# Performance work log

Measured on AMD Instinct MI355X. Metric: run time of the kernel, lower is better.

Reference implementation:

```python
import jax, jax.numpy as jnp
import numpy as np

WIN, OFFSET_D, TRUNC, SIGMA = 60, 40, 21, 9
EPS = 1e-8


def smoothing_filter():
    half = TRUNC // 2
    x = jnp.arange(-half, half + 1, dtype=jnp.float32)
    g = jnp.exp(-0.5 * (x / SIGMA) ** 2)
    g = g / g.sum()
    f = jnp.zeros(WIN, jnp.float32)
    c = WIN // 2
    return f.at[c - half:c + half + 1].set(g)


def setup_inputs() -> dict:
    key = jax.random.key(0)
    kx, kl, kt, kw = jax.random.split(key, 4)
    B, T, K = 64, 4000, 100
    X = jax.random.uniform(kx, (B, T, K), jnp.float32, 1e-4, 1.0 - 1e-4)
    lengths = jax.random.randint(kl, (B,), T // 2, T + 1, dtype=jnp.int32)
    tgt = jax.random.randint(kt, (B,), 0, K, dtype=jnp.int32)
    w_end = jax.random.randint(kw, (B,), 1, T // 2, dtype=jnp.int32)
    return {"X": X, "lengths": lengths, "tgt": tgt, "w_end": w_end}


def reference(X, lengths, tgt, w_end):
    B, T, K = X.shape
    filt = smoothing_filter()
    tau_s = jnp.maximum(0, w_end + OFFSET_D - WIN)      # (B,)
    tau_e = jnp.minimum(tau_s + WIN, lengths)           # (B,)
    t = jnp.arange(T)

    # ---- negative term: -log(1 - p) over all valid frames, excluding the
    # target keyword's pooling window [tau_s, tau_e) ----
    neg = -jnp.log(jnp.clip(1.0 - X, EPS, 1.0))                         # (B,T,K)
    len_mask = (t[None, :] < lengths[:, None]).astype(X.dtype)          # (B,T)
    win_mask = ((t[None, :] >= tau_s[:, None]) & (t[None, :] < tau_e[:, None])).astype(X.dtype)
    tgt_onehot = jax.nn.one_hot(tgt, K, dtype=X.dtype)                  # (B,K)
    neg_loss = jnp.sum(neg * len_mask[:, :, None]) - jnp.einsum('btk,bt,bk->', neg, win_mask, tgt_onehot)

    # ---- positive term: smoothed max pooling over window of target keyword ----
    prob_tgt = jnp.take_along_axis(X, tgt[:, None, None], axis=2)[..., 0]  # (B,T)
    win = jax.vmap(lambda p, s: jax.lax.dynamic_slice(p, (s,), (WIN,)))(prob_tgt, tau_s)
    Lw = tau_e - tau_s                                                   # valid window length
    pos = jnp.arange(WIN)
    valid = pos[None, :] < Lw[:, None]
    win = win * valid.astype(X.dtype)  # zero beyond valid length == zero-padded ragged conv
    total_pad = WIN - 1
    pl = total_pad // 2  # torch 'same': extra pad on the right
    smoothed = jax.lax.conv_general_dilated(
        win[:, None, :], filt[None, None, :], (1,), [(pl, total_pad - pl)])[:, 0, :]
    smoothed = jnp.clip(smoothed, EPS, 1.0)
    smoothed = jnp.where(valid, smoothed, 0.0)  # exclude out-of-window positions from max
    pos_loss = -jnp.log(smoothed.max(axis=1)).sum()

    return neg_loss + pos_loss
```

## Files before the change

kernel.cpp:

```cpp
#include <hip/hip_runtime.h>

#define WIN      60
#define OFFSET_D 40
#define TRUNC    21
#define EPS      1e-8f
#define BB       64
#define TT       4000
#define KK       100
#define TK       (TT*KK)
#define CHUNK    8192
#define CHB      49
#define NPART    (BB + BB*CHB)

__device__ __forceinline__ float clamp1(float x) {
    return fminf(fmaxf(1.0f - x, EPS), 1.0f);
}

__global__ __launch_bounds__(256) void fused_kernel(const float* __restrict__ X,
                                                    const int* __restrict__ lengths,
                                                    const int* __restrict__ tgt,
                                                    const int* __restrict__ w_end,
                                                    double* __restrict__ partials) {
    const int bid = blockIdx.x;

    if (bid >= BB) {
        const int nb   = bid - BB;
        const int b    = nb / CHB;
        const int c    = nb - b * CHB;
        const int s    = c * CHUNK;
        const int lenK = lengths[b] * KK;
        const float* __restrict__ base = X + (size_t)b * TK;

        float a0 = 0.f, a1 = 0.f, a2 = 0.f, a3 = 0.f;

        if (s + CHUNK <= lenK) {
            const float* __restrict__ p = base + s + (threadIdx.x << 2);
            float4 v[8];
            #pragma unroll
            for (int k = 0; k < 8; ++k)
                v[k] = *reinterpret_cast<const float4*>(p + k * 1024);
            #pragma unroll
            for (int k = 0; k < 8; ++k) {
                const float pr = (clamp1(v[k].x) * clamp1(v[k].y)) *
                                 (clamp1(v[k].z) * clamp1(v[k].w));
                ((k & 3) == 0 ? a0 : (k & 3) == 1 ? a1 : (k & 3) == 2 ? a2 : a3)
                    -= __logf(pr);
            }
        } else if (s < lenK) {
            const int e = min(s + CHUNK, lenK);
            for (int m = s + (threadIdx.x << 2); m < e; m += 256 * 4) {
                const float4 v = *reinterpret_cast<const float4*>(base + m);
                const float pr = (clamp1(v.x) * clamp1(v.y)) *
                                 (clamp1(v.z) * clamp1(v.w));
                a0 -= __logf(pr);
            }
        }
        float local = (a0 + a1) + (a2 + a3);

        #pragma unroll
        for (int off = 32; off > 0; off >>= 1) local += __shfl_down(local, off);
        __shared__ float wsum[4];
        if ((threadIdx.x & 63) == 0) wsum[threadIdx.x >> 6] = local;
        __syncthreads();
        if (threadIdx.x == 0)
            partials[bid] = (double)(wsum[0] + wsum[1] + wsum[2] + wsum[3]);
        return;
    }

    if (threadIdx.x >= 64) return;
    const int b   = bid;
    const int tid = threadIdx.x;

    const int ts = max(0, w_end[b] + OFFSET_D - WIN);
    const int te = min(ts + WIN, lengths[b]);
    const int Lw = te - ts;
    const int tg = tgt[b];

    float g = 0.0f;
    if (tid < TRUNC) {
        const float x = (tid - 10) * (1.0f / 9.0f);
        g = __expf(-0.5f * x * x);
    }
    float gs = g;
    #pragma unroll
    for (int off = 32; off > 0; off >>= 1) gs += __shfl_down(gs, off);
    gs = __shfl(gs, 0);
    const float gnorm = g / gs;

    float w = 0.0f, sub = 0.0f;
    if (tid < Lw) {
        const float xw = X[(size_t)b * TK + (size_t)(ts + tid) * KK + tg];
        w = xw;
        sub = -__logf(clamp1(xw));
    }

    float sm = 0.0f;
    #pragma unroll
    for (int u = 0; u < TRUNC; ++u) {
        const float gu = __shfl(gnorm, u);
        const int   j  = tid - 9 + u;
        const float wv = __shfl(w, j & 63);
        sm += gu * (((unsigned)j < (unsigned)WIN) ? wv : 0.0f);
    }

    float cand = (tid < Lw) ? fminf(fmaxf(sm, EPS), 1.0f) : 0.0f;
    #pragma unroll
    for (int off = 32; off > 0; off >>= 1) {
        sub  += __shfl_down(sub, off);
        cand  = fmaxf(cand, __shfl_down(cand, off));
    }
    if (tid == 0)
        partials[bid] = (double)(-__logf(cand) - sub);
}

__global__ __launch_bounds__(256) void finalize_kernel(const double* __restrict__ p,
                                                       float* __restrict__ out) {
    double s = 0.0;
    for (int i = threadIdx.x; i < NPART; i += 256) s += p[i];
    #pragma unroll
    for (int off = 32; off > 0; off >>= 1) s += __shfl_down(s, off);
    __shared__ double wsum[4];
    if ((threadIdx.x & 63) == 0) wsum[threadIdx.x >> 6] = s;
    __syncthreads();
    if (threadIdx.x == 0)
        out[0] = (float)(wsum[0] + wsum[1] + wsum[2] + wsum[3]);
}

extern "C" void kernel_launch(void* const* d_in, const int* in_sizes, int n_in,
                              void* d_out, int out_size, void* d_ws, size_t ws_size,
                              hipStream_t stream) {
    const float* X        = (const float*)d_in[0];
    const int*   lengths  = (const int*)d_in[1];
    const int*   tgt      = (const int*)d_in[2];
    const int*   w_end    = (const int*)d_in[3];
    float*       out      = (float*)d_out;
    double*      partials = (double*)d_ws;

    fused_kernel<<<BB + BB * CHB, 256, 0, stream>>>(X, lengths, tgt, w_end, partials);
    finalize_kernel<<<1, 256, 0, stream>>>(partials, out);
}
```

Measured before the change: 152.1 us.

## Fuse finalize via last-block atomic counter and double chunk size per block

Removes the separate finalize kernel launch. Each block writes its partial, increments an atomic counter, and the last block does the final sum. Chunk size per block doubles (fewer blocks, 16 float4 loads per thread), and the log calls are halved by multiplying two float4 products before each log. A hipMemsetAsync is added to reset the counter, and the merged product of 8 clamped values could underflow toward very small magnitudes.

```diff
diff --git a/kernel.cpp b/kernel.cpp
--- a/kernel.cpp
+++ b/kernel.cpp
@@ -8,9 +8,10 @@
 #define TT       4000
 #define KK       100
 #define TK       (TT*KK)
-#define CHUNK    8192
-#define CHB      49
-#define NPART    (BB + BB*CHB)
+#define CHUNK    16384
+#define CHB      25
+#define NNEG     (BB*CHB)
+#define NBLK     (BB + NNEG)
 
 __device__ __forceinline__ float clamp1(float x) {
     return fminf(fmaxf(1.0f - x, EPS), 1.0f);
@@ -20,8 +21,13 @@
                                                     const int* __restrict__ lengths,
                                                     const int* __restrict__ tgt,
                                                     const int* __restrict__ w_end,
-                                                    double* __restrict__ partials) {
+                                                    unsigned int* __restrict__ counter,
+                                                    double* __restrict__ partials,
+                                                    float* __restrict__ out) {
     const int bid = blockIdx.x;
+    const int tid = threadIdx.x;
+    double my_partial = 0.0;
+    bool have_partial = (tid == 0);
 
     if (bid >= BB) {
         const int nb   = bid - BB;
@@ -31,99 +37,112 @@
         const int lenK = lengths[b] * KK;
         const float* __restrict__ base = X + (size_t)b * TK;
 
-        float a0 = 0.f, a1 = 0.f, a2 = 0.f, a3 = 0.f;
+        float a0 = 0.f, a1 = 0.f;
 
         if (s + CHUNK <= lenK) {
-            const float* __restrict__ p = base + s + (threadIdx.x << 2);
-            float4 v[8];
+            const float* __restrict__ p = base + s + (tid << 2);
             #pragma unroll
-            for (int k = 0; k < 8; ++k)
-                v[k] = *reinterpret_cast<const float4*>(p + k * 1024);
-            #pragma unroll
-            for (int k = 0; k < 8; ++k) {
-                const float pr = (clamp1(v[k].x) * clamp1(v[k].y)) *
-                                 (clamp1(v[k].z) * clamp1(v[k].w));
-                ((k & 3) == 0 ? a0 : (k & 3) == 1 ? a1 : (k & 3) == 2 ? a2 : a3)
-                    -= __logf(pr);
+            for (int ph = 0; ph < 4; ++ph) {
+                float4 v[4];
+                #pragma unroll
+                for (int k = 0; k < 4; ++k)
+                    v[k] = *reinterpret_cast<const float4*>(p + (ph * 4 + k) * 1024);
+                const float pr0 = ((clamp1(v[0].x) * clamp1(v[0].y)) *
+                                   (clamp1(v[0].z) * clamp1(v[0].w))) *
+                                  ((clamp1(v[1].x) * clamp1(v[1].y)) *
+                                   (clamp1(v[1].z) * clamp1(v[1].w)));
+                const float pr1 = ((clamp1(v[2].x) * clamp1(v[2].y)) *
+                                   (clamp1(v[2].z) * clamp1(v[2].w))) *
+                                  ((clamp1(v[3].x) * clamp1(v[3].y)) *
+                                   (clamp1(v[3].z) * clamp1(v[3].w)));
+                a0 -= __logf(pr0);
+                a1 -= __logf(pr1);
             }
         } else if (s < lenK) {
-            const int e = min(s + CHUNK, lenK);
-            for (int m = s + (threadIdx.x << 2); m < e; m += 256 * 4) {
-                const float4 v = *reinterpret_cast<const float4*>(base + m);
-                const float pr = (clamp1(v.x) * clamp1(v.y)) *
-                                 (clamp1(v.z) * clamp1(v.w));
-                a0 -= __logf(pr);
+            const int m0 = s + (tid << 2);
+            #pragma unroll
+            for (int k = 0; k < 16; ++k) {
+                const int m = m0 + k * 1024;
+                if (m < lenK) {
+                    const float4 v = *reinterpret_cast<const float4*>(base + m);
+                    a0 -= __logf((clamp1(v.x) * clamp1(v.y)) *
+                                 (clamp1(v.z) * clamp1(v.w)));
+                }
             }
         }
-        float local = (a0 + a1) + (a2 + a3);
+        float local = a0 + a1;
 
         #pragma unroll
         for (int off = 32; off > 0; off >>= 1) local += __shfl_down(local, off);
         __shared__ float wsum[4];
-        if ((threadIdx.x & 63) == 0) wsum[threadIdx.x >> 6] = local;
+        if ((tid & 63) == 0) wsum[tid >> 6] = local;
         __syncthreads();
-        if (threadIdx.x == 0)
-            partials[bid] = (double)(wsum[0] + wsum[1] + wsum[2] + wsum[3]);
-        return;
+        if (tid == 0)
+            my_partial = (double)(wsum[0] + wsum[1] + wsum[2] + wsum[3]);
+    } else if (tid < 64) {
+        const int b  = bid;
+        const int ts = max(0, w_end[b] + OFFSET_D - WIN);
+        const int te = min(ts + WIN, lengths[b]);
+        const int Lw = te - ts;
+        const int tg = tgt[b];
+
+        float g = 0.0f;
+        if (tid < TRUNC) {
+            const float x = (tid - 10) * (1.0f / 9.0f);
+            g = __expf(-0.5f * x * x);
+        }
+        float gs = g;
+        #pragma unroll
+        for (int off = 32; off > 0; off >>= 1) gs += __shfl_down(gs, off);
+        gs = __shfl(gs, 0);
+        const float gnorm = g / gs;
+
+        float w = 0.0f, sub = 0.0f;
+        if (tid < Lw) {
+            const float xw = X[(size_t)b * TK + (size_t)(ts + tid) * KK + tg];
+            w = xw;
+            sub = -__logf(clamp1(xw));
+        }
+
+        float sm = 0.0f;
+        #pragma unroll
+        for (int u = 0; u < TRUNC; ++u) {
+            const float gu = __shfl(gnorm, u);
+            const int   j  = tid - 9 + u;
+            const float wv = __shfl(w, j & 63);
+            sm += gu * (((unsigned)j < (unsigned)WIN) ? wv : 0.0f);
+        }
+
+        float cand = (tid < Lw) ? fminf(fmaxf(sm, EPS), 1.0f) : 0.0f;
+        #pragma unroll
+        for (int off = 32; off > 0; off >>= 1) {
+            sub  += __shfl_down(sub, off);
+            cand  = fmaxf(cand, __shfl_down(cand, off));
+        }
+        if (tid == 0)
+            my_partial = (double)(-__logf(cand) - sub);
     }
 
-    if (threadIdx.x >= 64) return;
-    const int b   = bid;
-    const int tid = threadIdx.x;
+    __shared__ bool is_last;
+    if (have_partial) {
+        partials[bid] = my_partial;
+        __threadfence();
+        const unsigned int old = atomicAdd(counter, 1u);
+        is_last = (old == NBLK - 1);
+    }
+    __syncthreads();
+    if (!is_last) return;
+    __threadfence();
 
-    const int ts = max(0, w_end[b] + OFFSET_D - WIN);
-    const int te = min(ts + WIN, lengths[b]);
-    const int Lw = te - ts;
-    const int tg = tgt[b];
-
-    float g = 0.0f;
-    if (tid < TRUNC) {
-        const float x = (tid - 10) * (1.0f / 9.0f);
-        g = __expf(-0.5f * x * x);
-    }
-    float gs = g;
-    #pragma unroll
-    for (int off = 32; off > 0; off >>= 1) gs += __shfl_down(gs, off);
-    gs = __shfl(gs, 0);
-    const float gnorm = g / gs;
-
-    float w = 0.0f, sub = 0.0f;
-    if (tid < Lw) {
-        const float xw = X[(size_t)b * TK + (size_t)(ts + tid) * KK + tg];
-        w = xw;
-        sub = -__logf(clamp1(xw));
-    }
-
-    float sm = 0.0f;
-    #pragma unroll
-    for (int u = 0; u < TRUNC; ++u) {
-        const float gu = __shfl(gnorm, u);
-        const int   j  = tid - 9 + u;
-        const float wv = __shfl(w, j & 63);
-        sm += gu * (((unsigned)j < (unsigned)WIN) ? wv : 0.0f);
-    }
-
-    float cand = (tid < Lw) ? fminf(fmaxf(sm, EPS), 1.0f) : 0.0f;
-    #pragma unroll
-    for (int off = 32; off > 0; off >>= 1) {
-        sub  += __shfl_down(sub, off);
-        cand  = fmaxf(cand, __shfl_down(cand, off));
-    }
-    if (tid == 0)
-        partials[bid] = (double)(-__logf(cand) - sub);
-}
-
-__global__ __launch_bounds__(256) void finalize_kernel(const double* __restrict__ p,
-                                                       float* __restrict__ out) {
     double s = 0.0;
-    for (int i = threadIdx.x; i < NPART; i += 256) s += p[i];
+    for (int i = tid; i < NBLK; i += 256) s += partials[i];
     #pragma unroll
     for (int off = 32; off > 0; off >>= 1) s += __shfl_down(s, off);
-    __shared__ double wsum[4];
-    if ((threadIdx.x & 63) == 0) wsum[threadIdx.x >> 6] = s;
+    __shared__ double dsum[4];
+    if ((tid & 63) == 0) dsum[tid >> 6] = s;
     __syncthreads();
-    if (threadIdx.x == 0)
-        out[0] = (float)(wsum[0] + wsum[1] + wsum[2] + wsum[3]);
+    if (tid == 0)
+        out[0] = (float)(dsum[0] + dsum[1] + dsum[2] + dsum[3]);
 }
 
 extern "C" void kernel_launch(void* const* d_in, const int* in_sizes, int n_in,
@@ -134,8 +153,9 @@
     const int*   tgt      = (const int*)d_in[2];
     const int*   w_end    = (const int*)d_in[3];
     float*       out      = (float*)d_out;
-    double*      partials = (double*)d_ws;
+    unsigned int* counter = (unsigned int*)d_ws;
+    double*      partials = (double*)((char*)d_ws + 8);
 
-    fused_kernel<<<BB + BB * CHB, 256, 0, stream>>>(X, lengths, tgt, w_end, partials);
-    finalize_kernel<<<1, 256, 0, stream>>>(partials, out);
+    hipMemsetAsync(counter, 0, 8, stream);
+    fused_kernel<<<NBLK, 256, 0, stream>>>(X, lengths, tgt, w_end, counter, partials, out);
 }
```

New measurement: 232.6 us. +52.9%, slower.
